# Optimization experiments

Measured on AMD Instinct MI355X. Metric: run time of the kernel, lower is better.

The kernel has to match this reference:

```python
import jax, jax.numpy as jnp
import numpy as np

B, S, D = 1024, 256, 256  # batch, n_class, feature dim (g = n_component = 1)


def setup_inputs() -> dict:
    key = jax.random.key(0)
    k1, k2, k3 = jax.random.split(key, 3)
    x = jax.random.normal(k1, (B, D), dtype=jnp.float32)
    mu_p = jax.random.normal(k2, (S, 1, D), dtype=jnp.float32)
    sigma_p = jax.random.normal(k3, (S, 1, D, D), dtype=jnp.float32)
    return {"x": x, "mu_p": mu_p, "sigma_p": sigma_p}


def _log_probs(x, mu_p, sigma_p):
    sp = sigma_p[:, 0]            # (S, D, D), component index g=0
    mu = mu_p[:, 0]               # (S, D)
    # parameter_enforcing: m = sigma_p^T @ sigma_p (PSD);
    # mean of (real) eigenvalues of m == trace(m)/D, so the ridge term is
    # 0.01 * (trace(m)/D) * I, making sigma symmetric positive definite.
    m = jnp.einsum('skd,ske->sde', sp, sp)                      # (S, D, D)
    ridge = 0.01 * (jnp.trace(m, axis1=-2, axis2=-1) / D)       # (S,)
    sigma = m + ridge[:, None, None] * jnp.eye(D, dtype=m.dtype)
    # MVN log_prob via Cholesky: logdet = 2*sum(log diag L),
    # maha = || L^{-1} (x - mu) ||^2
    L = jnp.linalg.cholesky(sigma)                              # (S, D, D)
    logdet = 2.0 * jnp.sum(jnp.log(jnp.diagonal(L, axis1=-2, axis2=-1)), -1)  # (S,)
    diff = x[None, :, :] - mu[:, None, :]                       # (S, B, D)
    # batched triangular solve per class: y = L^{-1} diff^T -> (S, D, B)
    y = jax.vmap(lambda Ls, ds: jax.scipy.linalg.solve_triangular(Ls, ds.T, lower=True))(L, diff)
    maha = jnp.sum(y * y, axis=1)                               # (S, B)
    log2pi = jnp.log(2.0 * jnp.pi).astype(x.dtype)
    logp = -0.5 * (D * log2pi + logdet[:, None] + maha)         # (S, B)
    return logp.T                                               # (B, S)


def reference(x, mu_p, sigma_p):
    return _log_probs(x, mu_p, sigma_p)
```

## Files before the change

kernel.cpp:

```cpp
#include <hip/hip_runtime.h>
#include <math.h>


#define LOG2PI_D 470.4965290007924f
#define PS 68
#define PANEL (64*68)

typedef __attribute__((ext_vector_type(8))) short bf16x8;
typedef __attribute__((ext_vector_type(4))) float f32x4;

__device__ __forceinline__ unsigned bf16rtn(float f) {
  unsigned u = __float_as_uint(f);
  return (u + 0x7FFFu + ((u >> 16) & 1u)) >> 16;
}
__device__ __forceinline__ unsigned packhl(float v) {
  unsigned h = bf16rtn(v);
  float hf = __uint_as_float(h << 16);
  unsigned l = bf16rtn(v - hf);
  return (h << 16) | l;
}
__device__ __forceinline__ void hl2(float v0, float v1, unsigned& hw, unsigned& lw) {
  unsigned h0 = bf16rtn(v0), h1 = bf16rtn(v1);
  float r0 = v0 - __uint_as_float(h0 << 16);
  float r1 = v1 - __uint_as_float(h1 << 16);
  hw = h0 | (h1 << 16);
  lw = bf16rtn(r0) | (bf16rtn(r1) << 16);
}

__global__ __launch_bounds__(256) void k_gram(const float* __restrict__ sp,
                                              float* __restrict__ L,
                                              float* __restrict__ ridge_out) {
  __shared__ unsigned Hb[4 * 128 * 20];
  unsigned* AH = Hb;
  unsigned* AL = Hb + 128 * 20;
  unsigned* BH = Hb + 2 * 128 * 20;
  unsigned* BL = Hb + 3 * 128 * 20;
  int p = blockIdx.y, s = blockIdx.x;
  int bi = (p ? 128 : 0), bj = (p == 2 ? 128 : 0);
  const float* A = sp + (size_t)s * 65536;
  float* C = L + (size_t)s * 65536;
  int tid = threadIdx.x, w = tid >> 6, lane = tid & 63;
  int q = lane >> 4, n = lane & 15;
  int mt_[2] = {w, 7 - w};
  f32x4 acc[2][8] = {};
  int c = tid & 127, g = tid >> 7;

  float va[16], vb[16];
#pragma unroll
  for (int u = 0; u < 16; ++u) {
    va[u] = A[(size_t)(g * 16 + u) * 256 + bi + c];
    if (p == 1) vb[u] = A[(size_t)(g * 16 + u) * 256 + bj + c];
  }

  for (int ks = 0; ks < 8; ++ks) {
    __syncthreads();
    {
      unsigned hw[8], lw[8];
#pragma unroll
      for (int m = 0; m < 8; ++m) {
        float v0 = va[2 * m], v1 = va[2 * m + 1];
        unsigned h0 = bf16rtn(v0), h1 = bf16rtn(v1);
        float r0 = v0 - __uint_as_float(h0 << 16);
        float r1 = v1 - __uint_as_float(h1 << 16);
        hw[m] = h0 | (h1 << 16);
        lw[m] = bf16rtn(r0) | (bf16rtn(r1) << 16);
      }
      *(uint4*)&AH[c * 20 + g * 8] = make_uint4(hw[0], hw[1], hw[2], hw[3]);
      *(uint4*)&AH[c * 20 + g * 8 + 4] = make_uint4(hw[4], hw[5], hw[6], hw[7]);
      *(uint4*)&AL[c * 20 + g * 8] = make_uint4(lw[0], lw[1], lw[2], lw[3]);
      *(uint4*)&AL[c * 20 + g * 8 + 4] = make_uint4(lw[4], lw[5], lw[6], lw[7]);
      if (p == 1) {
#pragma unroll
        for (int m = 0; m < 8; ++m) {
          float v0 = vb[2 * m], v1 = vb[2 * m + 1];
          unsigned h0 = bf16rtn(v0), h1 = bf16rtn(v1);
          float r0 = v0 - __uint_as_float(h0 << 16);
          float r1 = v1 - __uint_as_float(h1 << 16);
          hw[m] = h0 | (h1 << 16);
          lw[m] = bf16rtn(r0) | (bf16rtn(r1) << 16);
        }
        *(uint4*)&BH[c * 20 + g * 8] = make_uint4(hw[0], hw[1], hw[2], hw[3]);
        *(uint4*)&BH[c * 20 + g * 8 + 4] = make_uint4(hw[4], hw[5], hw[6], hw[7]);
        *(uint4*)&BL[c * 20 + g * 8] = make_uint4(lw[0], lw[1], lw[2], lw[3]);
        *(uint4*)&BL[c * 20 + g * 8 + 4] = make_uint4(lw[4], lw[5], lw[6], lw[7]);
      }
    }
    __syncthreads();
    if (ks < 7) {
      int r0g = (ks + 1) * 32 + g * 16;
#pragma unroll
      for (int u = 0; u < 16; ++u) {
        va[u] = A[(size_t)(r0g + u) * 256 + bi + c];
        if (p == 1) vb[u] = A[(size_t)(r0g + u) * 256 + bj + c];
      }
    }
    const unsigned* TBH = (p == 1) ? BH : AH;
    const unsigned* TBL = (p == 1) ? BL : AL;
    bf16x8 Ah[2], Al[2];
#pragma unroll
    for (int t = 0; t < 2; ++t) {
      int col = mt_[t] * 16 + n;
      Ah[t] = *(const bf16x8*)&AH[col * 20 + q * 4];
      Al[t] = *(const bf16x8*)&AL[col * 20 + q * 4];
    }
    int ntmax = (p == 1) ? 8 : (8 - w);
    for (int nt = 0; nt < ntmax; ++nt) {
      bf16x8 bh = *(const bf16x8*)&TBH[(nt * 16 + n) * 20 + q * 4];
      bf16x8 bl = *(const bf16x8*)&TBL[(nt * 16 + n) * 20 + q * 4];
#pragma unroll
      for (int t = 0; t < 2; ++t) {
        if (p == 1 || nt <= mt_[t]) {
          acc[t][nt] = __builtin_amdgcn_mfma_f32_16x16x32_bf16(Ah[t], bh, acc[t][nt], 0, 0, 0);
          acc[t][nt] = __builtin_amdgcn_mfma_f32_16x16x32_bf16(Ah[t], bl, acc[t][nt], 0, 0, 0);
          acc[t][nt] = __builtin_amdgcn_mfma_f32_16x16x32_bf16(Al[t], bh, acc[t][nt], 0, 0, 0);
        }
      }
    }
  }
  if (p != 1) {
    float dsum = 0.f;
#pragma unroll
    for (int t = 0; t < 2; ++t) {
      if ((n >> 2) == q) dsum += acc[t][mt_[t]][n & 3];
    }
    dsum += __shfl_down(dsum, 32, 64);
    dsum += __shfl_down(dsum, 16, 64);
    dsum += __shfl_down(dsum, 8, 64);
    dsum += __shfl_down(dsum, 4, 64);
    dsum += __shfl_down(dsum, 2, 64);
    dsum += __shfl_down(dsum, 1, 64);
    if (lane == 0) atomicAdd(&ridge_out[s], dsum * (0.01f / 256.0f));
  }
  float* slab = (float*)Hb;
  for (int t = 0; t < 2; ++t) {
    __syncthreads();
#pragma unroll
    for (int nt = 0; nt < 8; ++nt)
#pragma unroll
      for (int r = 0; r < 4; ++r)
        slab[w * 2048 + (q * 4 + r) * 128 + nt * 16 + n] = acc[t][nt][r];
    __syncthreads();
#pragma unroll
    for (int it = 0; it < 8; ++it) {
      int idx = tid + it * 256;
      int row = idx >> 5, c4 = idx & 31;
      int wsrc = row >> 4, r16 = row & 15;
      int rt = t ? (7 - wsrc) : wsrc;
      if (p == 1 || (c4 >> 2) <= rt) {
        int d = bi + rt * 16 + r16;
        *(float4*)(C + (size_t)d * 256 + bj + c4 * 4) =
            *(float4*)&slab[wsrc * 2048 + r16 * 128 + c4 * 4];
      }
    }
  }
}

__global__ __launch_bounds__(1024) void k_factor(float* __restrict__ L,
                                                 const float* __restrict__ ridge_buf) {
  extern __shared__ float lds[];
  float* P = lds;
  float* W = lds + PANEL;
  float* WT = lds + 2 * PANEL;
  int s = blockIdx.x;
  float* M = L + (size_t)s * 65536;
  unsigned* M32 = (unsigned*)M;
  int tid = threadIdx.x;
  int k4 = tid & 15, r64 = tid >> 4;
  float ridge = ridge_buf[s];

  for (int kb = 0; kb < 4; ++kb) {
    int base = kb * 64;
    __syncthreads();
    if (kb == 0)
      *(float4*)&P[r64 * PS + k4 * 4] =
          *(const float4*)(M + (size_t)(base + r64) * 256 + base + k4 * 4);
    __syncthreads();
    if (tid < 64) P[tid * PS + tid] += ridge;
    __syncthreads();
    {
      int eo = tid & 63, ro = tid >> 6;
      for (int cb = 0; cb < 16; ++cb) {
        int c0 = cb * 4;
        float g00 = P[c0 * PS + c0];
        float g10 = P[(c0 + 1) * PS + c0], g11 = P[(c0 + 1) * PS + c0 + 1];
        float g20 = P[(c0 + 2) * PS + c0], g21 = P[(c0 + 2) * PS + c0 + 1],
              g22 = P[(c0 + 2) * PS + c0 + 2];
        float g30 = P[(c0 + 3) * PS + c0], g31 = P[(c0 + 3) * PS + c0 + 1],
              g32 = P[(c0 + 3) * PS + c0 + 2], g33 = P[(c0 + 3) * PS + c0 + 3];
        float l00 = sqrtf(g00), r0 = 1.f / l00;
        float l10 = g10 * r0, l20 = g20 * r0, l30 = g30 * r0;
        float l11 = sqrtf(g11 - l10 * l10), r1 = 1.f / l11;
        float l21 = (g21 - l20 * l10) * r1, l31 = (g31 - l30 * l10) * r1;
        float l22 = sqrtf(g22 - l20 * l20 - l21 * l21), r2 = 1.f / l22;
        float l32 = (g32 - l30 * l20 - l31 * l21) * r2;
        float l33 = sqrtf(g33 - l30 * l30 - l31 * l31 - l32 * l32), r3 = 1.f / l33;
        int e = c0 + 4 + eo;
        if (e < 64) {
          float p0 = P[e * PS + c0], p1 = P[e * PS + c0 + 1];
          float p2 = P[e * PS + c0 + 2], p3 = P[e * PS + c0 + 3];
          float le0 = p0 * r0;
          float le1 = (p1 - le0 * l10) * r1;
          float le2 = (p2 - le0 * l20 - le1 * l21) * r2;
          float le3 = (p3 - le0 * l30 - le1 * l31 - le2 * l32) * r3;
          for (int r = c0 + 4 + ro; r < 64; r += 16) {
            float q0 = P[r * PS + c0], q1 = P[r * PS + c0 + 1];
            float q2 = P[r * PS + c0 + 2], q3 = P[r * PS + c0 + 3];
            float lr0 = q0 * r0;
            float lr1 = (q1 - lr0 * l10) * r1;
            float lr2 = (q2 - lr0 * l20 - lr1 * l21) * r2;
            float lr3 = (q3 - lr0 * l30 - lr1 * l31 - lr2 * l32) * r3;
            P[r * PS + e] -= lr0 * le0 + lr1 * le1 + lr2 * le2 + lr3 * le3;
          }
        }
        __syncthreads();
      }
    }
    {
      int cb = tid >> 4, lane16 = tid & 15;
      int c0 = cb * 4;
      float vals[4][4];
      int rows[4], nr = 0;
      if (tid < 256) {
        float g00 = P[c0 * PS + c0];
        float g10 = P[(c0 + 1) * PS + c0], g11 = P[(c0 + 1) * PS + c0 + 1];
        float g20 = P[(c0 + 2) * PS + c0], g21 = P[(c0 + 2) * PS + c0 + 1],
              g22 = P[(c0 + 2) * PS + c0 + 2];
        float g30 = P[(c0 + 3) * PS + c0], g31 = P[(c0 + 3) * PS + c0 + 1],
              g32 = P[(c0 + 3) * PS + c0 + 2], g33 = P[(c0 + 3) * PS + c0 + 3];
        float l00 = sqrtf(g00), r0 = 1.f / l00;
        float l10 = g10 * r0, l20 = g20 * r0, l30 = g30 * r0;
        float l11 = sqrtf(g11 - l10 * l10), r1 = 1.f / l11;
        float l21 = (g21 - l20 * l10) * r1, l31 = (g31 - l30 * l10) * r1;
        float l22 = sqrtf(g22 - l20 * l20 - l21 * l21), r2 = 1.f / l22;
        float l32 = (g32 - l30 * l20 - l31 * l21) * r2;
        float l33 = sqrtf(g33 - l30 * l30 - l31 * l31 - l32 * l32), r3 = 1.f / l33;
        for (int r = c0 + lane16; r < 64; r += 16) {
          int i = r - c0;
          if (i == 0) { vals[nr][0] = l00; vals[nr][1] = 0; vals[nr][2] = 0; vals[nr][3] = 0; }
          else if (i == 1) { vals[nr][0] = l10; vals[nr][1] = l11; vals[nr][2] = 0; vals[nr][3] = 0; }
          else if (i == 2) { vals[nr][0] = l20; vals[nr][1] = l21; vals[nr][2] = l22; vals[nr][3] = 0; }
          else if (i == 3) { vals[nr][0] = l30; vals[nr][1] = l31; vals[nr][2] = l32; vals[nr][3] = l33; }
          else {
            float q0 = P[r * PS + c0], q1 = P[r * PS + c0 + 1];
            float q2 = P[r * PS + c0 + 2], q3 = P[r * PS + c0 + 3];
            float lr0 = q0 * r0;
            float lr1 = (q1 - lr0 * l10) * r1;
            float lr2 = (q2 - lr0 * l20 - lr1 * l21) * r2;
            float lr3 = (q3 - lr0 * l30 - lr1 * l31 - lr2 * l32) * r3;
            vals[nr][0] = lr0; vals[nr][1] = lr1; vals[nr][2] = lr2; vals[nr][3] = lr3;
          }
          rows[nr++] = r;
        }
      }
      __syncthreads();
      if (tid < 256) {
        for (int u = 0; u < nr; ++u) {
          int r = rows[u];
          P[r * PS + c0] = vals[u][0];
          P[r * PS + c0 + 1] = vals[u][1];
          P[r * PS + c0 + 2] = vals[u][2];
          P[r * PS + c0 + 3] = vals[u][3];
        }
      }
    }
    __syncthreads();
    for (int idx = tid; idx < PANEL; idx += 1024) W[idx] = 0.f;
    __syncthreads();
    for (int r8 = 0; r8 < 8; ++r8) {
      int k0 = r8 * 8;
      if (tid < 512) {
        int i = tid >> 6, cc = tid & 63;
        int row = k0 + i;
        float ss = 0.f;
        for (int k = 0; k < k0; ++k) ss += P[row * PS + k] * W[k * PS + cc];
        WT[i * PS + cc] = ss;
      }
      __syncthreads();
      if (tid < 64) {
        int cc = tid;
        float x[8];
#pragma unroll
        for (int m = 0; m < 8; ++m) {
          float v = ((cc == k0 + m) ? 1.f : 0.f) - WT[m * PS + cc];
#pragma unroll
          for (int u = 0; u < 8; ++u)
            if (u < m) v -= P[(k0 + m) * PS + k0 + u] * x[u];
          x[m] = v / P[(k0 + m) * PS + k0 + m];
          W[(k0 + m) * PS + cc] = x[m];
        }
      }
      __syncthreads();
    }
    {
      float4 v = *(float4*)&W[r64 * PS + k4 * 4];
      WT[(k4 * 4 + 0) * PS + r64] = v.x;
      WT[(k4 * 4 + 1) * PS + r64] = v.y;
      WT[(k4 * 4 + 2) * PS + r64] = v.z;
      WT[(k4 * 4 + 3) * PS + r64] = v.w;
    }
    __syncthreads();
    *(float4*)(M + (size_t)(base + r64) * 256 + base + k4 * 4) = *(float4*)&W[r64 * PS + k4 * 4];
    int nrt = 3 - kb;
    for (int rt0 = 0; rt0 < nrt; rt0 += 2) {
      int pr = tid >> 9, t2 = tid & 511;
      int my = rt0 + pr;
      bool act = my < nrt;
      float* Tb = lds + (size_t)(3 + (act ? my : 0)) * PANEL;
      int k42 = t2 & 15, rbl = t2 >> 4;
      int ty2 = t2 >> 4, tx2 = t2 & 15;
      int g0 = base + 64 + my * 64;
      __syncthreads();
      if (act) {
#pragma unroll
        for (int r = rbl; r < 64; r += 32) {
          float4 v = *(const float4*)(M + (size_t)(g0 + r) * 256 + base + k42 * 4);
          Tb[(k42 * 4 + 0) * PS + r] = v.x;
          Tb[(k42 * 4 + 1) * PS + r] = v.y;
          Tb[(k42 * 4 + 2) * PS + r] = v.z;
          Tb[(k42 * 4 + 3) * PS + r] = v.w;
        }
      }
      __syncthreads();
      float acc[2][4] = {};
      if (act) {
        for (int k = 0; k < 64; ++k) {
          float a0 = Tb[k * PS + ty2 * 2], a1 = Tb[k * PS + ty2 * 2 + 1];
          float b[4];
          *(float4*)b = *(float4*)&WT[k * PS + tx2 * 4];
#pragma unroll
          for (int j = 0; j < 4; ++j) {
            acc[0][j] += a0 * b[j];
            acc[1][j] += a1 * b[j];
          }
        }
      }
      __syncthreads();
      if (act) {
#pragma unroll
        for (int i = 0; i < 2; ++i)
#pragma unroll
          for (int j = 0; j < 4; ++j) Tb[(tx2 * 4 + j) * PS + ty2 * 2 + i] = acc[i][j];
      }
      __syncthreads();
      if (act) {
#pragma unroll
        for (int r = rbl; r < 64; r += 32)
          *(float4*)(M + (size_t)(base + r) * 256 + g0 + k42 * 4) = *(float4*)&Tb[r * PS + k42 * 4];
      }
    }
    __syncthreads();
    int np = ((3 - kb) * (4 - kb)) / 2;
    for (int p0 = 0; p0 < np; p0 += 2) {
      int pr = tid >> 9, t2 = tid & 511;
      int my = p0 + pr;
      bool act = my < np;
      int ti = kb + 1, tj = kb + 1;
      {
        int cnt = 0;
        for (int a = kb + 1; a < 4; ++a)
          for (int b = kb + 1; b <= a; ++b) {
            if (cnt == my) { ti = a; tj = b; }
            ++cnt;
          }
      }
      float* Pi = lds + (size_t)(3 + (ti - kb - 1)) * PANEL;
      float* Pj = lds + (size_t)(3 + (tj - kb - 1)) * PANEL;
      int ty2 = t2 >> 4, tx2 = t2 & 15;
      float acc[2][4];
      if (act) {
#pragma unroll
        for (int i = 0; i < 2; ++i)
          *(float4*)&acc[i][0] =
              *(const float4*)(M + (size_t)(ti * 64 + ty2 * 2 + i) * 256 + tj * 64 + tx2 * 4);
        for (int k = 0; k < 64; ++k) {
          float a0 = Pi[k * PS + ty2 * 2], a1 = Pi[k * PS + ty2 * 2 + 1];
          float b[4];
          *(float4*)b = *(float4*)&Pj[k * PS + tx2 * 4];
#pragma unroll
          for (int j = 0; j < 4; ++j) {
            acc[0][j] -= a0 * b[j];
            acc[1][j] -= a1 * b[j];
          }
        }
        if (ti == tj && ti == kb + 1) {
#pragma unroll
          for (int i = 0; i < 2; ++i)
            *(float4*)&P[(ty2 * 2 + i) * PS + tx2 * 4] =
                make_float4(acc[i][0], acc[i][1], acc[i][2], acc[i][3]);
        } else {
#pragma unroll
          for (int i = 0; i < 2; ++i)
            *(float4*)(M + (size_t)(ti * 64 + ty2 * 2 + i) * 256 + tj * 64 + tx2 * 4) =
                make_float4(acc[i][0], acc[i][1], acc[i][2], acc[i][3]);
        }
      }
    }
  }

  {
    unsigned* U = (unsigned*)lds;
    const int ST = 36, HL = 2304, PP = 4608;
    const int PA = 3 * PP, PC = 4 * PP;
    int lane = tid & 63, wv = tid >> 6;
    int q = lane >> 4, n = lane & 15;
    int wr = wv >> 2, wc = wv & 3;
    int pc = tid & 63, pg = tid >> 6;
    int colA = wr * 16 + n, colB = wc * 16 + n;

    for (int j = 0; j < 3; ++j) {
      __syncthreads();
      {
        float v0 = M[(size_t)(j * 64 + pg * 4 + 0) * 256 + j * 64 + pc];
        float v1 = M[(size_t)(j * 64 + pg * 4 + 1) * 256 + j * 64 + pc];
        float v2 = M[(size_t)(j * 64 + pg * 4 + 2) * 256 + j * 64 + pc];
        float v3 = M[(size_t)(j * 64 + pg * 4 + 3) * 256 + j * 64 + pc];
        unsigned hw, lw;
        hl2(v0, v1, hw, lw);
        U[pc * ST + 2 * pg] = hw; U[HL + pc * ST + 2 * pg] = lw;
        hl2(v2, v3, hw, lw);
        U[pc * ST + 2 * pg + 1] = hw; U[HL + pc * ST + 2 * pg + 1] = lw;
      }
      for (int i = j + 1; i < 4; ++i) {
        f32x4 a1 = {0.f, 0.f, 0.f, 0.f};
        for (int kk = j; kk < i; ++kk) {
          __syncthreads();
          {
            float v0 = M[(size_t)(kk * 64 + pg * 4 + 0) * 256 + i * 64 + pc];
            float v1 = M[(size_t)(kk * 64 + pg * 4 + 1) * 256 + i * 64 + pc];
            float v2 = M[(size_t)(kk * 64 + pg * 4 + 2) * 256 + i * 64 + pc];
            float v3 = M[(size_t)(kk * 64 + pg * 4 + 3) * 256 + i * 64 + pc];
            unsigned hw, lw;
            hl2(v0, v1, hw, lw);
            U[PA + pc * ST + 2 * pg] = hw; U[PA + HL + pc * ST + 2 * pg] = lw;
            hl2(v2, v3, hw, lw);
            U[PA + pc * ST + 2 * pg + 1] = hw; U[PA + HL + pc * ST + 2 * pg + 1] = lw;
          }
          __syncthreads();
          int PB = (kk - j) * PP;
#pragma unroll
          for (int ks = 0; ks < 2; ++ks) {
            bf16x8 Ah = *(const bf16x8*)&U[PA + colA * ST + ks * 16 + q * 4];
            bf16x8 Al = *(const bf16x8*)&U[PA + HL + colA * ST + ks * 16 + q * 4];
            bf16x8 Bh = *(const bf16x8*)&U[PB + colB * ST + ks * 16 + q * 4];
            bf16x8 Bl = *(const bf16x8*)&U[PB + HL + colB * ST + ks * 16 + q * 4];
            a1 = __builtin_amdgcn_mfma_f32_16x16x32_bf16(Ah, Bh, a1, 0, 0, 0);
            a1 = __builtin_amdgcn_mfma_f32_16x16x32_bf16(Ah, Bl, a1, 0, 0, 0);
            a1 = __builtin_amdgcn_mfma_f32_16x16x32_bf16(Al, Bh, a1, 0, 0, 0);
          }
        }
        __syncthreads();
        {
          float4 v = *(const float4*)(M + (size_t)(i * 64 + pc) * 256 + i * 64 + pg * 4);
          unsigned hw, lw;
          hl2(v.x, v.y, hw, lw);
          U[PA + pc * ST + 2 * pg] = hw; U[PA + HL + pc * ST + 2 * pg] = lw;
          hl2(v.z, v.w, hw, lw);
          U[PA + pc * ST + 2 * pg + 1] = hw; U[PA + HL + pc * ST + 2 * pg + 1] = lw;
        }
        {
          unsigned hw, lw;
          hl2(a1[0], a1[1], hw, lw);
          U[PC + colB * ST + wr * 8 + 2 * q] = hw;
          U[PC + HL + colB * ST + wr * 8 + 2 * q] = lw;
          hl2(a1[2], a1[3], hw, lw);
          U[PC + colB * ST + wr * 8 + 2 * q + 1] = hw;
          U[PC + HL + colB * ST + wr * 8 + 2 * q + 1] = lw;
        }
        __syncthreads();
        f32x4 a2 = {0.f, 0.f, 0.f, 0.f};
#pragma unroll
        for (int ks = 0; ks < 2; ++ks) {
          bf16x8 Ah = *(const bf16x8*)&U[PA + colA * ST + ks * 16 + q * 4];
          bf16x8 Al = *(const bf16x8*)&U[PA + HL + colA * ST + ks * 16 + q * 4];
          bf16x8 Bh = *(const bf16x8*)&U[PC + colB * ST + ks * 16 + q * 4];
          bf16x8 Bl = *(const bf16x8*)&U[PC + HL + colB * ST + ks * 16 + q * 4];
          a2 = __builtin_amdgcn_mfma_f32_16x16x32_bf16(Ah, Bh, a2, 0, 0, 0);
          a2 = __builtin_amdgcn_mfma_f32_16x16x32_bf16(Ah, Bl, a2, 0, 0, 0);
          a2 = __builtin_amdgcn_mfma_f32_16x16x32_bf16(Al, Bh, a2, 0, 0, 0);
        }
        float dv[4] = {-a2[0], -a2[1], -a2[2], -a2[3]};
#pragma unroll
        for (int r = 0; r < 4; ++r)
          M32[(size_t)(i * 64 + wr * 16 + q * 4 + r) * 256 + j * 64 + colB] = packhl(dv[r]);
        if (i < 3) {
          int PB = (i - j) * PP;
          unsigned hw, lw;
          hl2(dv[0], dv[1], hw, lw);
          U[PB + colB * ST + wr * 8 + 2 * q] = hw;
          U[PB + HL + colB * ST + wr * 8 + 2 * q] = lw;
          hl2(dv[2], dv[3], hw, lw);
          U[PB + colB * ST + wr * 8 + 2 * q + 1] = hw;
          U[PB + HL + colB * ST + wr * 8 + 2 * q + 1] = lw;
        }
      }
    }
  }
}

__global__ __launch_bounds__(512) void k_maha(const float* __restrict__ x,
                                              const float* __restrict__ mu_p,
                                              const float* __restrict__ Lw,
                                              float* __restrict__ out) {
  __shared__ __align__(16) short Bh[128 * 40];
  __shared__ __align__(16) short Bl[128 * 40];
  __shared__ float Red[1025];
  int s = blockIdx.x, b0 = blockIdx.y * 128;
  const float* Mf = Lw + (size_t)s * 65536;
  const unsigned* M32 = (const unsigned*)Mf;
  int tid = threadIdx.x, w = tid >> 6, lane = tid & 63;
  int q = lane >> 4, n = lane & 15;
  int mt_[2] = {w, 15 - w};
  f32x4 acc[2][8] = {};

  for (int ks = 0; ks < 8; ++ks) {
    __syncthreads();
    {
      int b = tid >> 2, q8 = tid & 3;
      const float* xp = x + (size_t)(b0 + b) * 256 + ks * 32 + q8 * 8;
      const float* mp = mu_p + (size_t)s * 256 + ks * 32 + q8 * 8;
      float4 xa = ((const float4*)xp)[0], xb = ((const float4*)xp)[1];
      float4 ma = ((const float4*)mp)[0], mb = ((const float4*)mp)[1];
      float dv[8] = {xa.x - ma.x, xa.y - ma.y, xa.z - ma.z, xa.w - ma.w,
                     xb.x - mb.x, xb.y - mb.y, xb.z - mb.z, xb.w - mb.w};
      unsigned h[8], l[8];
#pragma unroll
      for (int jj = 0; jj < 8; ++jj) {
        h[jj] = bf16rtn(dv[jj]);
        float hf = __uint_as_float(h[jj] << 16);
        l[jj] = bf16rtn(dv[jj] - hf);
      }
      *(uint4*)&Bh[b * 40 + q8 * 8] =
          make_uint4(h[0] | (h[1] << 16), h[2] | (h[3] << 16),
                     h[4] | (h[5] << 16), h[6] | (h[7] << 16));
      *(uint4*)&Bl[b * 40 + q8 * 8] =
          make_uint4(l[0] | (l[1] << 16), l[2] | (l[3] << 16),
                     l[4] | (l[5] << 16), l[6] | (l[7] << 16));
    }
    __syncthreads();
    bf16x8 Ah[2], Al[2];
    bool act[2];
#pragma unroll
    for (int t = 0; t < 2; ++t) {
      int mt = mt_[t];
      act[t] = ks < ((mt + 2) >> 1);
      if (act[t]) {
        const unsigned* ap = M32 + (size_t)(mt * 16 + n) * 256 + ks * 32 + q * 8;
        uint4 u0 = *(const uint4*)ap;
        uint4 u1 = *(const uint4*)(ap + 4);
        unsigned uu[8] = {u0.x, u0.y, u0.z, u0.w, u1.x, u1.y, u1.z, u1.w};
        if ((ks >> 1) == (mt >> 2)) {
#pragma unroll
          for (int jj = 0; jj < 8; ++jj) {
            float f = __uint_as_float(uu[jj]);
            unsigned hh = bf16rtn(f);
            float hf = __uint_as_float(hh << 16);
            Ah[t][jj] = (short)hh;
            Al[t][jj] = (short)bf16rtn(f - hf);
          }
        } else {
#pragma unroll
          for (int jj = 0; jj < 8; ++jj) {
            Ah[t][jj] = (short)(uu[jj] >> 16);
            Al[t][jj] = (short)(uu[jj] & 0xffffu);
          }
        }
      }
    }
#pragma unroll
    for (int bsub = 0; bsub < 8; ++bsub) {
      bf16x8 bh = *(const bf16x8*)&Bh[(bsub * 16 + n) * 40 + q * 8];
      bf16x8 bl = *(const bf16x8*)&Bl[(bsub * 16 + n) * 40 + q * 8];
#pragma unroll
      for (int t = 0; t < 2; ++t) {
        if (act[t]) {
          acc[t][bsub] = __builtin_amdgcn_mfma_f32_16x16x32_bf16(Ah[t], bh, acc[t][bsub], 0, 0, 0);
          acc[t][bsub] = __builtin_amdgcn_mfma_f32_16x16x32_bf16(Ah[t], bl, acc[t][bsub], 0, 0, 0);
          acc[t][bsub] = __builtin_amdgcn_mfma_f32_16x16x32_bf16(Al[t], bh, acc[t][bsub], 0, 0, 0);
        }
      }
    }
  }
#pragma unroll
  for (int bsub = 0; bsub < 8; ++bsub) {
    float v = 0.f;
#pragma unroll
    for (int t = 0; t < 2; ++t)
#pragma unroll
      for (int r = 0; r < 4; ++r) v += acc[t][bsub][r] * acc[t][bsub][r];
    v += __shfl_xor(v, 16, 64);
    v += __shfl_xor(v, 32, 64);
    if (lane < 16) Red[w * 128 + bsub * 16 + lane] = v;
  }
  if (w == 0) {
    float ld = 0.f;
#pragma unroll
    for (int c = 0; c < 4; ++c)
      ld += logf(Mf[(size_t)(c * 64 + lane) * 256 + c * 64 + lane]);
    ld += __shfl_down(ld, 32, 64);
    ld += __shfl_down(ld, 16, 64);
    ld += __shfl_down(ld, 8, 64);
    ld += __shfl_down(ld, 4, 64);
    ld += __shfl_down(ld, 2, 64);
    ld += __shfl_down(ld, 1, 64);
    if (lane == 0) Red[1024] = ld;
  }
  __syncthreads();
  if (tid < 128) {
    float mh = 0.f;
#pragma unroll
    for (int w2 = 0; w2 < 8; ++w2) mh += Red[w2 * 128 + tid];
    out[(size_t)(b0 + tid) * 256 + s] = -0.5f * (LOG2PI_D - 2.0f * Red[1024] + mh);
  }
}

extern "C" void kernel_launch(void* const* d_in, const int* in_sizes, int n_in,
                              void* d_out, int out_size, void* d_ws, size_t ws_size,
                              hipStream_t stream) {
  const float* x = (const float*)d_in[0];
  const float* mu = (const float*)d_in[1];
  const float* sp = (const float*)d_in[2];
  float* out = (float*)d_out;
  float* L = (float*)d_ws;

  const int fact_lds = 6 * PANEL * 4;
  (void)hipFuncSetAttribute((const void*)k_factor,
                            hipFuncAttributeMaxDynamicSharedMemorySize, fact_lds);

  k_gram<<<dim3(256, 3), 256, 0, stream>>>(sp, L, out);
  k_factor<<<256, 1024, fact_lds, stream>>>(L, out);
  k_maha<<<dim3(256, 8), 512, 0, stream>>>(x, mu, L, out);
}
```

Measured before the change: 534.5 us.

## Shrink k_factor LDS footprint to four panels for higher occupancy

Cuts the factorization kernel's dynamic shared memory from six panels to four. It does this by dropping the transposed W copy, reading W column-wise directly in the triangular-update GEMM, and reusing the P panel and the two remaining scratch panels for trailing tiles. The inverse phase now keeps one block fragment in registers (d2hold) so it only needs two B-panel slots. Launch bounds are raised to ask for more resident blocks per CU. The cost is strided, bank-conflicting LDS reads of W, extra syncs, and more register pressure.

```diff
diff --git a/kernel.cpp b/kernel.cpp
--- a/kernel.cpp
+++ b/kernel.cpp
@@ -155,12 +155,13 @@
   }
 }
 
-__global__ __launch_bounds__(1024) void k_factor(float* __restrict__ L,
-                                                 const float* __restrict__ ridge_buf) {
+__global__ __launch_bounds__(1024, 8) void k_factor(float* __restrict__ L,
+                                                    const float* __restrict__ ridge_buf) {
   extern __shared__ float lds[];
   float* P = lds;
   float* W = lds + PANEL;
-  float* WT = lds + 2 * PANEL;
+  float* T0p = lds + 2 * PANEL;
+  float* T1p = lds + 3 * PANEL;
   int s = blockIdx.x;
   float* M = L + (size_t)s * 65536;
   unsigned* M32 = (unsigned*)M;
@@ -273,7 +274,7 @@
         int row = k0 + i;
         float ss = 0.f;
         for (int k = 0; k < k0; ++k) ss += P[row * PS + k] * W[k * PS + cc];
-        WT[i * PS + cc] = ss;
+        T0p[i * PS + cc] = ss;
       }
       __syncthreads();
       if (tid < 64) {
@@ -281,7 +282,7 @@
         float x[8];
 #pragma unroll
         for (int m = 0; m < 8; ++m) {
-          float v = ((cc == k0 + m) ? 1.f : 0.f) - WT[m * PS + cc];
+          float v = ((cc == k0 + m) ? 1.f : 0.f) - T0p[m * PS + cc];
 #pragma unroll
           for (int u = 0; u < 8; ++u)
             if (u < m) v -= P[(k0 + m) * PS + k0 + u] * x[u];
@@ -291,21 +292,13 @@
       }
       __syncthreads();
     }
-    {
-      float4 v = *(float4*)&W[r64 * PS + k4 * 4];
-      WT[(k4 * 4 + 0) * PS + r64] = v.x;
-      WT[(k4 * 4 + 1) * PS + r64] = v.y;
-      WT[(k4 * 4 + 2) * PS + r64] = v.z;
-      WT[(k4 * 4 + 3) * PS + r64] = v.w;
-    }
-    __syncthreads();
     *(float4*)(M + (size_t)(base + r64) * 256 + base + k4 * 4) = *(float4*)&W[r64 * PS + k4 * 4];
     int nrt = 3 - kb;
     for (int rt0 = 0; rt0 < nrt; rt0 += 2) {
       int pr = tid >> 9, t2 = tid & 511;
       int my = rt0 + pr;
       bool act = my < nrt;
-      float* Tb = lds + (size_t)(3 + (act ? my : 0)) * PANEL;
+      float* Tb = (my == 2) ? P : (my == 1 ? T1p : T0p);
       int k42 = t2 & 15, rbl = t2 >> 4;
       int ty2 = t2 >> 4, tx2 = t2 & 15;
       int g0 = base + 64 + my * 64;
@@ -324,13 +317,12 @@
       float acc[2][4] = {};
       if (act) {
         for (int k = 0; k < 64; ++k) {
-          float a0 = Tb[k * PS + ty2 * 2], a1 = Tb[k * PS + ty2 * 2 + 1];
-          float b[4];
-          *(float4*)b = *(float4*)&WT[k * PS + tx2 * 4];
-#pragma unroll
-          for (int j = 0; j < 4; ++j) {
-            acc[0][j] += a0 * b[j];
-            acc[1][j] += a1 * b[j];
+          float a0 = Tb[k * PS + ty2 * 2], a1v = Tb[k * PS + ty2 * 2 + 1];
+#pragma unroll
+          for (int jj = 0; jj < 4; ++jj) {
+            float bw = W[(tx2 * 4 + jj) * PS + k];
+            acc[0][jj] += a0 * bw;
+            acc[1][jj] += a1v * bw;
           }
         }
       }
@@ -357,15 +349,16 @@
       int ti = kb + 1, tj = kb + 1;
       {
         int cnt = 0;
-        for (int a = kb + 1; a < 4; ++a)
+        for (int a = 3; a >= kb + 1; --a)
           for (int b = kb + 1; b <= a; ++b) {
             if (cnt == my) { ti = a; tj = b; }
             ++cnt;
           }
       }
-      float* Pi = lds + (size_t)(3 + (ti - kb - 1)) * PANEL;
-      float* Pj = lds + (size_t)(3 + (tj - kb - 1)) * PANEL;
+      float* Pi = (kb == 0 && ti == 3) ? P : ((ti - kb - 1) ? T1p : T0p);
+      float* Pj = (kb == 0 && tj == 3) ? P : ((tj - kb - 1) ? T1p : T0p);
       int ty2 = t2 >> 4, tx2 = t2 & 15;
+      __syncthreads();
       float acc[2][4];
       if (act) {
 #pragma unroll
@@ -373,13 +366,13 @@
           *(float4*)&acc[i][0] =
               *(const float4*)(M + (size_t)(ti * 64 + ty2 * 2 + i) * 256 + tj * 64 + tx2 * 4);
         for (int k = 0; k < 64; ++k) {
-          float a0 = Pi[k * PS + ty2 * 2], a1 = Pi[k * PS + ty2 * 2 + 1];
+          float a0 = Pi[k * PS + ty2 * 2], a1v = Pi[k * PS + ty2 * 2 + 1];
           float b[4];
           *(float4*)b = *(float4*)&Pj[k * PS + tx2 * 4];
 #pragma unroll
           for (int j = 0; j < 4; ++j) {
             acc[0][j] -= a0 * b[j];
-            acc[1][j] -= a1 * b[j];
+            acc[1][j] -= a1v * b[j];
           }
         }
         if (ti == tj && ti == kb + 1) {
@@ -400,97 +393,93 @@
   {
     unsigned* U = (unsigned*)lds;
     const int ST = 36, HL = 2304, PP = 4608;
-    const int PA = 3 * PP, PC = 4 * PP;
+    const int PB0 = 0, PB1 = PP, PA = 2 * PP, PC = 3 * PP;
     int lane = tid & 63, wv = tid >> 6;
     int q = lane >> 4, n = lane & 15;
     int wr = wv >> 2, wc = wv & 3;
     int pc = tid & 63, pg = tid >> 6;
     int colA = wr * 16 + n, colB = wc * 16 + n;
 
+    auto pack4 = [&](int dst, float v0, float v1, float v2, float v3) {
+      unsigned hw, lw;
+      hl2(v0, v1, hw, lw);
+      U[dst + pc * ST + 2 * pg] = hw;
+      U[dst + HL + pc * ST + 2 * pg] = lw;
+      hl2(v2, v3, hw, lw);
+      U[dst + pc * ST + 2 * pg + 1] = hw;
+      U[dst + HL + pc * ST + 2 * pg + 1] = lw;
+    };
+    auto packfrag = [&](const float* dv, int dst) {
+      unsigned hw, lw;
+      hl2(dv[0], dv[1], hw, lw);
+      U[dst + colB * ST + wr * 8 + 2 * q] = hw;
+      U[dst + HL + colB * ST + wr * 8 + 2 * q] = lw;
+      hl2(dv[2], dv[3], hw, lw);
+      U[dst + colB * ST + wr * 8 + 2 * q + 1] = hw;
+      U[dst + HL + colB * ST + wr * 8 + 2 * q + 1] = lw;
+    };
+    auto mm3 = [&](int pa, int pb, f32x4& a) {
+#pragma unroll
+      for (int ks2 = 0; ks2 < 2; ++ks2) {
+        bf16x8 Ah = *(const bf16x8*)&U[pa + colA * ST + ks2 * 16 + q * 4];
+        bf16x8 Al = *(const bf16x8*)&U[pa + HL + colA * ST + ks2 * 16 + q * 4];
+        bf16x8 Bh = *(const bf16x8*)&U[pb + colB * ST + ks2 * 16 + q * 4];
+        bf16x8 Bl = *(const bf16x8*)&U[pb + HL + colB * ST + ks2 * 16 + q * 4];
+        a = __builtin_amdgcn_mfma_f32_16x16x32_bf16(Ah, Bh, a, 0, 0, 0);
+        a = __builtin_amdgcn_mfma_f32_16x16x32_bf16(Ah, Bl, a, 0, 0, 0);
+        a = __builtin_amdgcn_mfma_f32_16x16x32_bf16(Al, Bh, a, 0, 0, 0);
+      }
+    };
+
+    float d2hold[4] = {0.f, 0.f, 0.f, 0.f};
     for (int j = 0; j < 3; ++j) {
       __syncthreads();
-      {
-        float v0 = M[(size_t)(j * 64 + pg * 4 + 0) * 256 + j * 64 + pc];
-        float v1 = M[(size_t)(j * 64 + pg * 4 + 1) * 256 + j * 64 + pc];
-        float v2 = M[(size_t)(j * 64 + pg * 4 + 2) * 256 + j * 64 + pc];
-        float v3 = M[(size_t)(j * 64 + pg * 4 + 3) * 256 + j * 64 + pc];
-        unsigned hw, lw;
-        hl2(v0, v1, hw, lw);
-        U[pc * ST + 2 * pg] = hw; U[HL + pc * ST + 2 * pg] = lw;
-        hl2(v2, v3, hw, lw);
-        U[pc * ST + 2 * pg + 1] = hw; U[HL + pc * ST + 2 * pg + 1] = lw;
-      }
+      pack4(PB0,
+            M[(size_t)(j * 64 + pg * 4 + 0) * 256 + j * 64 + pc],
+            M[(size_t)(j * 64 + pg * 4 + 1) * 256 + j * 64 + pc],
+            M[(size_t)(j * 64 + pg * 4 + 2) * 256 + j * 64 + pc],
+            M[(size_t)(j * 64 + pg * 4 + 3) * 256 + j * 64 + pc]);
       for (int i = j + 1; i < 4; ++i) {
         f32x4 a1 = {0.f, 0.f, 0.f, 0.f};
         for (int kk = j; kk < i; ++kk) {
+          int bsel = kk - j;
+          if (j == 0 && i == 3 && kk == 2) {
+            __syncthreads();
+            packfrag(d2hold, PB1);
+            bsel = 1;
+          }
           __syncthreads();
-          {
-            float v0 = M[(size_t)(kk * 64 + pg * 4 + 0) * 256 + i * 64 + pc];
-            float v1 = M[(size_t)(kk * 64 + pg * 4 + 1) * 256 + i * 64 + pc];
-            float v2 = M[(size_t)(kk * 64 + pg * 4 + 2) * 256 + i * 64 + pc];
-            float v3 = M[(size_t)(kk * 64 + pg * 4 + 3) * 256 + i * 64 + pc];
-            unsigned hw, lw;
-            hl2(v0, v1, hw, lw);
-            U[PA + pc * ST + 2 * pg] = hw; U[PA + HL + pc * ST + 2 * pg] = lw;
-            hl2(v2, v3, hw, lw);
-            U[PA + pc * ST + 2 * pg + 1] = hw; U[PA + HL + pc * ST + 2 * pg + 1] = lw;
-          }
+          pack4(PA,
+                M[(size_t)(kk * 64 + pg * 4 + 0) * 256 + i * 64 + pc],
+                M[(size_t)(kk * 64 + pg * 4 + 1) * 256 + i * 64 + pc],
+                M[(size_t)(kk * 64 + pg * 4 + 2) * 256 + i * 64 + pc],
+                M[(size_t)(kk * 64 + pg * 4 + 3) * 256 + i * 64 + pc]);
           __syncthreads();
-          int PB = (kk - j) * PP;
-#pragma unroll
-          for (int ks = 0; ks < 2; ++ks) {
-            bf16x8 Ah = *(const bf16x8*)&U[PA + colA * ST + ks * 16 + q * 4];
-            bf16x8 Al = *(const bf16x8*)&U[PA + HL + colA * ST + ks * 16 + q * 4];
-            bf16x8 Bh = *(const bf16x8*)&U[PB + colB * ST + ks * 16 + q * 4];
-            bf16x8 Bl = *(const bf16x8*)&U[PB + HL + colB * ST + ks * 16 + q * 4];
-            a1 = __builtin_amdgcn_mfma_f32_16x16x32_bf16(Ah, Bh, a1, 0, 0, 0);
-            a1 = __builtin_amdgcn_mfma_f32_16x16x32_bf16(Ah, Bl, a1, 0, 0, 0);
-            a1 = __builtin_amdgcn_mfma_f32_16x16x32_bf16(Al, Bh, a1, 0, 0, 0);
-          }
+          mm3(PA, (bsel == 0) ? PB0 : PB1, a1);
         }
         __syncthreads();
         {
           float4 v = *(const float4*)(M + (size_t)(i * 64 + pc) * 256 + i * 64 + pg * 4);
-          unsigned hw, lw;
-          hl2(v.x, v.y, hw, lw);
-          U[PA + pc * ST + 2 * pg] = hw; U[PA + HL + pc * ST + 2 * pg] = lw;
-          hl2(v.z, v.w, hw, lw);
-          U[PA + pc * ST + 2 * pg + 1] = hw; U[PA + HL + pc * ST + 2 * pg + 1] = lw;
+          pack4(PA, v.x, v.y, v.z, v.w);
         }
         {
-          unsigned hw, lw;
-          hl2(a1[0], a1[1], hw, lw);
-          U[PC + colB * ST + wr * 8 + 2 * q] = hw;
-          U[PC + HL + colB * ST + wr * 8 + 2 * q] = lw;
-          hl2(a1[2], a1[3], hw, lw);
-          U[PC + colB * ST + wr * 8 + 2 * q + 1] = hw;
-          U[PC + HL + colB * ST + wr * 8 + 2 * q + 1] = lw;
+          float c4[4] = {a1[0], a1[1], a1[2], a1[3]};
+          packfrag(c4, PC);
         }
         __syncthreads();
         f32x4 a2 = {0.f, 0.f, 0.f, 0.f};
-#pragma unroll
-        for (int ks = 0; ks < 2; ++ks) {
-          bf16x8 Ah = *(const bf16x8*)&U[PA + colA * ST + ks * 16 + q * 4];
-          bf16x8 Al = *(const bf16x8*)&U[PA + HL + colA * ST + ks * 16 + q * 4];
-          bf16x8 Bh = *(const bf16x8*)&U[PC + colB * ST + ks * 16 + q * 4];
-          bf16x8 Bl = *(const bf16x8*)&U[PC + HL + colB * ST + ks * 16 + q * 4];
-          a2 = __builtin_amdgcn_mfma_f32_16x16x32_bf16(Ah, Bh, a2, 0, 0, 0);
-          a2 = __builtin_amdgcn_mfma_f32_16x16x32_bf16(Ah, Bl, a2, 0, 0, 0);
-          a2 = __builtin_amdgcn_mfma_f32_16x16x32_bf16(Al, Bh, a2, 0, 0, 0);
-        }
+        mm3(PA, PC, a2);
         float dv[4] = {-a2[0], -a2[1], -a2[2], -a2[3]};
 #pragma unroll
         for (int r = 0; r < 4; ++r)
           M32[(size_t)(i * 64 + wr * 16 + q * 4 + r) * 256 + j * 64 + colB] = packhl(dv[r]);
         if (i < 3) {
-          int PB = (i - j) * PP;
-          unsigned hw, lw;
-          hl2(dv[0], dv[1], hw, lw);
-          U[PB + colB * ST + wr * 8 + 2 * q] = hw;
-          U[PB + HL + colB * ST + wr * 8 + 2 * q] = lw;
-          hl2(dv[2], dv[3], hw, lw);
-          U[PB + colB * ST + wr * 8 + 2 * q + 1] = hw;
-          U[PB + HL + colB * ST + wr * 8 + 2 * q + 1] = lw;
+          if (j == 0 && i == 2) {
+            d2hold[0] = dv[0]; d2hold[1] = dv[1];
+            d2hold[2] = dv[2]; d2hold[3] = dv[3];
+          } else {
+            packfrag(dv, PB1);
+          }
         }
       }
     }
@@ -622,7 +611,7 @@
   float* out = (float*)d_out;
   float* L = (float*)d_ws;
 
-  const int fact_lds = 6 * PANEL * 4;
+  const int fact_lds = 4 * 4608 * 4;
   (void)hipFuncSetAttribute((const void*)k_factor,
                             hipFuncAttributeMaxDynamicSharedMemorySize, fact_lds);
 
```

Result: slower. 646.2 us (+20.9%).
